# Performance work log

Hardware: AMD Instinct MI355X
Metric: run time of the kernel (lower is better)

The kernel has to match this reference:

```python
import jax, jax.numpy as jnp
import numpy as np


def silu(x):
    return x * jax.nn.sigmoid(x)


def setup_inputs() -> dict:
    key = jax.random.key(0)
    ks = jax.random.split(key, 16)
    b, n, k, d0, d1, hid = 2, 4096, 32, 64, 32, 32
    edge_in_dim = d0 * 2 + d1 + 1  # 161
    std = 1e-3  # init_eps normal init for Linear weights

    features0 = jax.random.normal(ks[0], (b, n, d0, 1), jnp.float32)
    features1 = jax.random.normal(ks[1], (b, n, d1, 3), jnp.float32)
    neighbor_indices = jax.random.randint(ks[2], (b, n, k), 0, n)
    neighbor_masks = jax.random.randint(ks[3], (b, n, k), 0, 2).astype(bool)
    rel_dist = jax.random.uniform(ks[4], (b, n, k), jnp.float32)

    def lin(kk, i, o):
        return std * jax.random.normal(kk, (i, o), jnp.float32)

    params = dict(
        W_e1=lin(ks[5], edge_in_dim, edge_in_dim * 2), b_e1=jnp.zeros(edge_in_dim * 2, jnp.float32),
        W_e2=lin(ks[6], edge_in_dim * 2, hid), b_e2=jnp.zeros(hid, jnp.float32),
        W_h1=lin(ks[7], hid, hid * 4), b_h1=jnp.zeros(hid * 4, jnp.float32),
        W_h2=lin(ks[8], hid * 4, d1), b_h2=jnp.zeros(d1, jnp.float32),
        W_n1=lin(ks[9], d0 + hid, d0 * 2), b_n1=jnp.zeros(d0 * 2, jnp.float32),
        W_n2=lin(ks[10], d0 * 2, d0), b_n2=jnp.zeros(d0, jnp.float32),
        W_g=lin(ks[11], d0, d1), b_g=jnp.zeros(d1, jnp.float32),
        ln_g=jnp.ones(d0, jnp.float32), ln_b=jnp.zeros(d0, jnp.float32),
        hn_scale=jnp.full((1, 1, 1, d1, 1), 0.01, jnp.float32),
        hn_bias=jnp.full((1, 1, 1, d1, 1), 0.01, jnp.float32),
    )
    return dict(features0=features0, features1=features1,
                neighbor_indices=neighbor_indices, neighbor_masks=neighbor_masks,
                rel_dist=rel_dist, **params)


def reference(features0, features1, neighbor_indices, neighbor_masks, rel_dist,
              W_e1, b_e1, W_e2, b_e2, W_h1, b_h1, W_h2, b_h2,
              W_n1, b_n1, W_n2, b_n2, W_g, b_g, ln_g, ln_b, hn_scale, hn_bias):
    b, n, k = neighbor_indices.shape
    bi = jnp.arange(b)[:, None, None]

    nodes = features0[..., 0]                                   # [b,n,d0]
    # gather neighbor higher-type features; rel_htype at selected pairs only
    h_j = features1[bi, neighbor_indices]                       # [b,n,k,d1,3]
    rel = features1[:, :, None, :, :] - h_j                     # [b,n,k,d1,3]
    rel_norm = jnp.linalg.norm(rel, axis=-1)                    # [b,n,k,d1]

    nodes_j = nodes[bi, neighbor_indices]                       # [b,n,k,d0]
    nodes_i = jnp.broadcast_to(nodes[:, :, None, :], nodes_j.shape)
    edge_in = jnp.concatenate([nodes_i, nodes_j, rel_norm, rel_dist[..., None]], axis=-1)

    m_ij = silu(silu(edge_in @ W_e1 + b_e1) @ W_e2 + b_e2)      # [b,n,k,hid]
    # NOTE: original splits htype_weights BEFORE masked_fill, so weights are unmasked
    w = silu(m_ij @ W_h1 + b_h1) @ W_h2 + b_h2                  # [b,n,k,d1]

    nrm = rel_norm[..., None]
    normed_rel = rel / jnp.clip(nrm, 1e-8) * (nrm * hn_scale + hn_bias)
    htype_update = jnp.einsum('bijdm,bijd->bidm', normed_rel, w)  # [b,n,d1,3]

    m_ij = jnp.where(neighbor_masks[..., None], m_ij, 0.0)
    m_i = m_ij.sum(axis=-2)                                     # [b,n,hid]

    mu = nodes.mean(-1, keepdims=True)
    var = nodes.var(-1, keepdims=True)
    normed_nodes = (nodes - mu) / jnp.sqrt(var + 1e-5) * ln_g + ln_b

    node_in = jnp.concatenate([normed_nodes, m_i], axis=-1)
    node_out = silu(node_in @ W_n1 + b_n1) @ W_n2 + b_n2 + nodes

    gate = jax.nn.sigmoid(node_out @ W_g + b_g)                 # [b,n,d1]
    f1_out = (features1 + htype_update) * gate[..., None]
    return node_out[..., None], f1_out
```

## Files before the change

### kernel.cpp

```cpp
#include <hip/hip_runtime.h>
#include <math.h>

#define NN_ 4096

typedef __attribute__((ext_vector_type(4))) float f4_t;
typedef __attribute__((ext_vector_type(2))) long l2_t;

__device__ __forceinline__ unsigned short f2bf(float x) {
    union { float f; unsigned u; } v; v.f = x;
    unsigned r = v.u + 0x7fffu + ((v.u >> 16) & 1u);
    return (unsigned short)(r >> 16);
}
__device__ __forceinline__ float bf2f(unsigned short h) {
    union { unsigned u; float f; } v; v.u = ((unsigned)h) << 16;
    return v.f;
}

__device__ __forceinline__ unsigned char sw_enc_fp8(float x) {
    if (x != x) return 0x7f;
    unsigned s = (x < 0.f) ? 0x80u : 0u;
    float a = fabsf(x);
    if (a >= 448.f) return (unsigned char)(s | 0x7e);
    int e; frexpf(a, &e); e -= 1;
    if (e < -6) e = -6;
    float scaled = ldexpf(a, 3 - e);
    int qq = (int)lrintf(scaled);
    if (qq >= 16) { qq = 8; e += 1; if (e > 8) return (unsigned char)(s | 0x7e); }
    if (qq < 8) return (unsigned char)(s | (unsigned)qq);
    return (unsigned char)(s | (unsigned)((e + 7) << 3) | (unsigned)(qq - 8));
}
__device__ __forceinline__ float sw_dec_fp8(unsigned char b) {
    int s = b >> 7, ef = (b >> 3) & 0xf, m = b & 7;
    float v = ef ? ldexpf((float)(8 + m), ef - 10) : ldexpf((float)m, -9);
    return s ? -v : v;
}
__device__ __forceinline__ unsigned pack4_fp8(float a, float b, float c, float d) {
#if __has_builtin(__builtin_amdgcn_cvt_pk_fp8_f32)
    int v = __builtin_amdgcn_cvt_pk_fp8_f32(a, b, 0, false);
    v = __builtin_amdgcn_cvt_pk_fp8_f32(c, d, v, true);
    return (unsigned)v;
#else
    return (unsigned)sw_enc_fp8(a) | ((unsigned)sw_enc_fp8(b) << 8) |
           ((unsigned)sw_enc_fp8(c) << 16) | ((unsigned)sw_enc_fp8(d) << 24);
#endif
}
__device__ __forceinline__ unsigned char enc_fp8(float a) {
#if __has_builtin(__builtin_amdgcn_cvt_pk_fp8_f32)
    return (unsigned char)(__builtin_amdgcn_cvt_pk_fp8_f32(a, 0.f, 0, false) & 0xff);
#else
    return sw_enc_fp8(a);
#endif
}
__device__ __forceinline__ float dec_fp8(unsigned char b) {
#if __has_builtin(__builtin_amdgcn_cvt_f32_fp8)
    return __builtin_amdgcn_cvt_f32_fp8((int)b, 0);
#else
    return sw_dec_fp8(b);
#endif
}
__device__ __forceinline__ f4_t mfma_fp8(long a, long b, f4_t c) {
    return __builtin_amdgcn_mfma_f32_16x16x32_fp8_fp8(a, b, c, 0, 0, 0);
}

__device__ __forceinline__ float silu_ps(float x, float S) {
    float x2 = x * x;
    float t = __builtin_fmaf(x2, -(S * (1.f / 48.f)), S * 0.25f);
    float s = __builtin_fmaf(x, t, S * 0.5f);
    return x * s;
}

#define WS_E2 67584
#define WS_H1 79872
#define WS_H2 83968
#define WS_N1 88064
#define WS_N2 100352
#define WS_G  108544
#define WS_END 110592

__global__ void __launch_bounds__(256) cvt_w(
    const float* __restrict__ W_e1, const float* __restrict__ W_e2,
    const float* __restrict__ W_h1, const float* __restrict__ W_h2,
    const float* __restrict__ W_n1, const float* __restrict__ W_n2,
    const float* __restrict__ W_g,  unsigned char* __restrict__ ws)
{
    int gid = blockIdx.x * 256 + threadIdx.x;
    if (gid >= WS_END) return;
    float v = 0.f;
    if (gid < WS_E2) {
        int t = gid / 3072, r = gid - t * 3072;
        int lane = r / 48; r -= lane * 48;
        int kc = r >> 3, b = r & 7;
        int n = t * 16 + (lane & 15), k = kc * 32 + (lane >> 4) * 8 + b;
        if (n < 322 && k < 161) v = W_e1[k * 322 + n];
    } else if (gid < WS_H1) {
        int g2 = gid - WS_E2;
        int mt = g2 / 6144; g2 -= mt * 6144;
        int lane = g2 / 96; g2 -= lane * 96;
        int s = g2 >> 3, b = g2 & 7;
        if (s < 11) {
            int n = mt * 16 + (lane & 15), k = s * 32 + (lane >> 4) * 8 + b;
            if (k < 322) v = W_e2[k * 32 + n];
        }
    } else if (gid < WS_H2) {
        int g2 = gid - WS_H1;
        int ng = g2 >> 11; g2 &= 2047;
        int lane = g2 >> 5, i = (g2 >> 3) & 3, b = g2 & 7;
        int n = (ng * 4 + i) * 16 + (lane & 15), k = (lane >> 4) * 8 + b;
        v = W_h1[k * 128 + n];
    } else if (gid < WS_N1) {
        int g2 = gid - WS_H2;
        int nt = g2 >> 11; g2 &= 2047;
        int lane = g2 >> 5, kc = (g2 >> 3) & 3, b = g2 & 7;
        int n = nt * 16 + (lane & 15), k = kc * 32 + (lane >> 4) * 8 + b;
        v = W_h2[k * 32 + n];
    } else if (gid < WS_N2) {
        int g2 = gid - WS_N1;
        int nt = g2 / 1536; g2 -= nt * 1536;
        int lane = g2 / 24; g2 -= lane * 24;
        int kc = g2 >> 3, b = g2 & 7;
        int n = nt * 16 + (lane & 15), k = kc * 32 + (lane >> 4) * 8 + b;
        v = W_n1[k * 128 + n];
    } else if (gid < WS_G) {
        int g2 = gid - WS_N2;
        int nt = g2 >> 11; g2 &= 2047;
        int lane = g2 >> 5, kc = (g2 >> 3) & 3, b = g2 & 7;
        int n = nt * 16 + (lane & 15), k = kc * 32 + (lane >> 4) * 8 + b;
        v = W_n2[k * 64 + n];
    } else {
        int g2 = gid - WS_G;
        int nt = g2 >> 10; g2 &= 1023;
        int lane = g2 >> 4, kc = (g2 >> 3) & 1, b = g2 & 7;
        int n = nt * 16 + (lane & 15), k = kc * 32 + (lane >> 4) * 8 + b;
        v = W_g[k * 32 + n];
    }
    ws[gid] = enc_fp8(v * 256.f);
}

__global__ void __launch_bounds__(256, 5) egnn_edge(
    const float* __restrict__ f0, const float* __restrict__ f1,
    const int* __restrict__ nidx, const int* __restrict__ nmsk,
    const float* __restrict__ rdist,
    const unsigned char* __restrict__ wbf,
    const float* __restrict__ b_e1, const float* __restrict__ b_e2,
    const float* __restrict__ b_h1, const float* __restrict__ b_h2,
    const float* __restrict__ hs,   const float* __restrict__ hb,
    float* __restrict__ out0, float* __restrict__ out1)
{
    __shared__ __align__(16) unsigned char R1[23040];
    __shared__ __align__(16) unsigned char R2[6144];
    __shared__ __align__(16) unsigned char R3[2560];
    __shared__ int s_jj[64];

    const int tid  = threadIdx.x;
    const int blk  = blockIdx.x;
    const int bb   = blk >> 11;
    const int wave = tid >> 6, lane = tid & 63;
    const int q    = lane >> 4, l16 = lane & 15;

    unsigned long long ball = 0;
    if (wave == 0) {
        int mv = nmsk[(size_t)blk * 64 + lane];
        ball = __ballot(mv != 0);
    }

    {
        const int e = tid >> 2, r = tid & 2 ? (tid & 3) : (tid & 3);
        const int rr4 = tid & 3;
        const int jj = nidx[(size_t)blk * 64 + e];
        if (rr4 == 0) s_jj[e] = jj;
        const int node = blk * 2 + (e >> 5);
        const float* ni = f0 + (size_t)node * 64;
        const float* nj = f0 + ((size_t)(bb * NN_ + jj)) * 64;
        const float* fi = f1 + (size_t)node * 96;
        const float* fj = f1 + ((size_t)(bb * NN_ + jj)) * 96;
        unsigned char* einp = R1 + e * 216;

        {
            float4 v0 = *(const float4*)(ni + 16 * rr4);
            float4 v1 = *(const float4*)(ni + 16 * rr4 + 4);
            float4 v2 = *(const float4*)(ni + 16 * rr4 + 8);
            float4 v3 = *(const float4*)(ni + 16 * rr4 + 12);
            uint2 w;
            w.x = pack4_fp8(v0.x, v0.y, v0.z, v0.w);
            w.y = pack4_fp8(v1.x, v1.y, v1.z, v1.w);
            *(uint2*)(einp + 16 * rr4) = w;
            w.x = pack4_fp8(v2.x, v2.y, v2.z, v2.w);
            w.y = pack4_fp8(v3.x, v3.y, v3.z, v3.w);
            *(uint2*)(einp + 16 * rr4 + 8) = w;
        }
        {
            float4 v0 = *(const float4*)(nj + 16 * rr4);
            float4 v1 = *(const float4*)(nj + 16 * rr4 + 4);
            float4 v2 = *(const float4*)(nj + 16 * rr4 + 8);
            float4 v3 = *(const float4*)(nj + 16 * rr4 + 12);
            uint2 w;
            w.x = pack4_fp8(v0.x, v0.y, v0.z, v0.w);
            w.y = pack4_fp8(v1.x, v1.y, v1.z, v1.w);
            *(uint2*)(einp + 64 + 16 * rr4) = w;
            w.x = pack4_fp8(v2.x, v2.y, v2.z, v2.w);
            w.y = pack4_fp8(v3.x, v3.y, v3.z, v3.w);
            *(uint2*)(einp + 64 + 16 * rr4 + 8) = w;
        }
        {
            float rl[24];
            #pragma unroll
            for (int s = 0; s < 6; s++) {
                float4 a = *(const float4*)(fi + 24 * rr4 + 4 * s);
                float4 c = *(const float4*)(fj + 24 * rr4 + 4 * s);
                rl[4*s+0] = a.x - c.x; rl[4*s+1] = a.y - c.y;
                rl[4*s+2] = a.z - c.z; rl[4*s+3] = a.w - c.w;
            }
            uint2* rdst = (uint2*)(R2 + e * 96 + 24 * rr4);
            uint2 u;
            u.x = pack4_fp8(rl[0], rl[1], rl[2],  rl[3]);
            u.y = pack4_fp8(rl[4], rl[5], rl[6],  rl[7]);
            rdst[0] = u;
            u.x = pack4_fp8(rl[8],  rl[9],  rl[10], rl[11]);
            u.y = pack4_fp8(rl[12], rl[13], rl[14], rl[15]);
            rdst[1] = u;
            u.x = pack4_fp8(rl[16], rl[17], rl[18], rl[19]);
            u.y = pack4_fp8(rl[20], rl[21], rl[22], rl[23]);
            rdst[2] = u;
            float nr[8];
            #pragma unroll
            for (int t = 0; t < 8; t++)
                nr[t] = __builtin_amdgcn_sqrtf(
                    __builtin_fmaf(rl[3*t], rl[3*t],
                    __builtin_fmaf(rl[3*t+1], rl[3*t+1], rl[3*t+2]*rl[3*t+2])));
            uint2 nw;
            nw.x = pack4_fp8(nr[0], nr[1], nr[2], nr[3]);
            nw.y = pack4_fp8(nr[4], nr[5], nr[6], nr[7]);
            *(uint2*)(einp + 128 + 8 * rr4) = nw;
        }
        if (rr4 == 0) {
            float rdv = rdist[(size_t)blk * 64 + e];
            uint2 w; w.x = pack4_fp8(rdv, 0.f, 0.f, 0.f); w.y = 0u;
            *(uint2*)(einp + 160) = w;
        } else {
            uint2 z; z.x = 0u; z.y = 0u;
            *(uint2*)(einp + 160 + 8 * rr4) = z;
        }
    }
    __syncthreads();

    long be[4][6];
    #pragma unroll
    for (int nt = 0; nt < 4; nt++) {
        const unsigned char* bp = R1 + ((nt * 16 + l16)) * 216 + q * 8;
        #pragma unroll
        for (int kc = 0; kc < 6; kc++)
            be[nt][kc] = *(const long*)(bp + kc * 32);
    }
    __syncthreads();

    for (int t = wave; t < 22; t += 4) {
        const unsigned char* wp = wbf + (size_t)t * 3072 + lane * 48;
        l2_t w0 = *(const l2_t*)(wp);
        l2_t w1 = *(const l2_t*)(wp + 16);
        l2_t w2 = *(const l2_t*)(wp + 32);
        long af[6] = {w0.x, w0.y, w1.x, w1.y, w2.x, w2.y};
        f4_t a0 = (f4_t)0.f, a1 = (f4_t)0.f, a2 = (f4_t)0.f, a3 = (f4_t)0.f;
        #pragma unroll
        for (int kc = 0; kc < 6; kc++) {
            a0 = mfma_fp8(af[kc], be[0][kc], a0);
            a1 = mfma_fp8(af[kc], be[1][kc], a1);
            a2 = mfma_fp8(af[kc], be[2][kc], a2);
            a3 = mfma_fp8(af[kc], be[3][kc], a3);
        }
        const int c0 = t * 16 + q * 4;
        float bv[4];
        if (c0 + 3 < 322) {
            float4 b4 = *(const float4*)(b_e1 + c0);
            bv[0] = b4.x; bv[1] = b4.y; bv[2] = b4.z; bv[3] = b4.w;
        } else {
            #pragma unroll
            for (int i = 0; i < 4; i++) bv[i] = (c0 + i < 322) ? b_e1[c0 + i] : 0.f;
        }
        #pragma unroll
        for (int nt = 0; nt < 4; nt++) {
            f4_t aa = nt == 0 ? a0 : (nt == 1 ? a1 : (nt == 2 ? a2 : a3));
            float y[4];
            #pragma unroll
            for (int i = 0; i < 4; i++) {
                float x = __builtin_fmaf(aa[i], 1.f / 256.f, bv[i]);
                y[i] = x * __builtin_fmaf(x, 16.f, 32.f);
            }
            *(unsigned*)(R1 + (nt * 16 + l16) * 360 + c0) =
                pack4_fp8(y[0], y[1], y[2], y[3]);
        }
    }
    __syncthreads();

    {
        const int mt2 = wave & 1;
        const unsigned char* wp2 = wbf + WS_E2 + mt2 * 6144 + lane * 96;
        long wf2[11];
        #pragma unroll
        for (int p = 0; p < 5; p++) {
            l2_t u = *(const l2_t*)(wp2 + p * 16);
            wf2[2 * p] = u.x; wf2[2 * p + 1] = u.y;
        }
        wf2[10] = *(const long*)(wp2 + 80);
        int h0 = mt2 * 16 + q * 4;
        float4 b4 = *(const float4*)(b_e2 + h0);
        float bvv[4] = {b4.x, b4.y, b4.z, b4.w};
        #pragma unroll
        for (int half = 0; half < 2; half++) {
            const int ntile = (wave >> 1) + half * 2;
            long ba[11];
            const unsigned char* apb = R1 + (ntile * 16 + l16) * 360 + q * 8;
            #pragma unroll
            for (int kc = 0; kc < 11; kc++) ba[kc] = *(const long*)(apb + kc * 32);
            f4_t m0 = (f4_t)0.f;
            #pragma unroll
            for (int kc = 0; kc < 11; kc++)
                m0 = mfma_fp8(wf2[kc], ba[kc], m0);
            const int e = ntile * 16 + l16;
            float y[4];
            #pragma unroll
            for (int i = 0; i < 4; i++) {
                float x = __builtin_fmaf(m0[i], 1.f / 16384.f, bvv[i]);
                y[i] = x * __builtin_fmaf(x, 2048.f, 4096.f);
            }
            *(unsigned*)(R3 + e * 40 + h0) = pack4_fp8(y[0], y[1], y[2], y[3]);
        }
    }
    __syncthreads();

    {
        const int em = wave;
        long am = *(const long*)(R3 + (em * 16 + l16) * 40 + q * 8);
        #pragma unroll
        for (int ng = 0; ng < 2; ng++) {
            const unsigned char* hp = wbf + WS_H1 + ng * 2048 + lane * 32;
            l2_t hv0 = *(const l2_t*)hp;
            l2_t hv1 = *(const l2_t*)(hp + 16);
            long bw[4] = {hv0.x, hv0.y, hv1.x, hv1.y};
            #pragma unroll
            for (int i = 0; i < 4; i++) {
                int nt = ng * 4 + i;
                f4_t a3 = mfma_fp8(am, bw[i], (f4_t)0.f);
                int c = nt * 16 + l16;
                float bv = b_h1[c];
                #pragma unroll
                for (int rr = 0; rr < 4; rr++) {
                    int e = em * 16 + q * 4 + rr;
                    float zh = __builtin_fmaf(a3[rr], 1.f / 2097152.f, bv);
                    R1[e * 152 + c] = enc_fp8(silu_ps(zh, 4194304.f));
                }
            }
        }
    }
    __syncthreads();

    {
        const int em = wave;
        const unsigned char* ap = R1 + (em * 16 + l16) * 152 + q * 8;
        long aq[4];
        #pragma unroll
        for (int kc = 0; kc < 4; kc++) aq[kc] = *(const long*)(ap + kc * 32);
        unsigned short* wfp = (unsigned short*)(R1 + 16384);
        #pragma unroll
        for (int nt2 = 0; nt2 < 2; nt2++) {
            const unsigned char* wp = wbf + WS_H2 + nt2 * 2048 + lane * 32;
            l2_t wv0 = *(const l2_t*)wp;
            l2_t wv1 = *(const l2_t*)(wp + 16);
            f4_t cc = (f4_t)0.f;
            cc = mfma_fp8(aq[0], wv0.x, cc);
            cc = mfma_fp8(aq[1], wv0.y, cc);
            cc = mfma_fp8(aq[2], wv1.x, cc);
            cc = mfma_fp8(aq[3], wv1.y, cc);
            int d = nt2 * 16 + l16;
            float bv = b_h2[d], hss = hs[d], hbb = hb[d];
            #pragma unroll
            for (int rr = 0; rr < 4; rr++) {
                int e = em * 16 + q * 4 + rr;
                float r0 = dec_fp8(R2[e * 96 + 3 * d + 0]);
                float r1 = dec_fp8(R2[e * 96 + 3 * d + 1]);
                float r2 = dec_fp8(R2[e * 96 + 3 * d + 2]);
                float nr = __builtin_amdgcn_sqrtf(
                    __builtin_fmaf(r0, r0, __builtin_fmaf(r1, r1, r2 * r2)));
                float fac = __builtin_fmaf(nr, hss, hbb) *
                            __builtin_amdgcn_rcpf(fmaxf(nr, 1e-8f));
                float wout = __builtin_fmaf(cc[rr], 1.f / 1073741824.f, bv);
                wfp[e * 36 + d] = f2bf(wout * fac);
            }
        }
    }
    __syncthreads();

    const unsigned short* wfp = (const unsigned short*)(R1 + 16384);
    #pragma unroll
    for (int sel = 0; sel < 2; sel++) {
        const int node = blk * 2 + sel;
        if (wave == 0) {
            const int hq = lane & 7, g = lane >> 3;
            float a0 = 0.f, a1 = 0.f, a2 = 0.f, a3 = 0.f;
            #pragma unroll
            for (int it = 0; it < 4; it++) {
                int e = sel * 32 + g * 4 + it;
                float mf = ((ball >> e) & 1ull) ? 1.f : 0.f;
                unsigned m4 = *(const unsigned*)(R3 + e * 40 + hq * 4);
                a0 = __builtin_fmaf(mf, dec_fp8((unsigned char)(m4 & 0xff)), a0);
                a1 = __builtin_fmaf(mf, dec_fp8((unsigned char)((m4 >> 8) & 0xff)), a1);
                a2 = __builtin_fmaf(mf, dec_fp8((unsigned char)((m4 >> 16) & 0xff)), a2);
                a3 = __builtin_fmaf(mf, dec_fp8((unsigned char)(m4 >> 24)), a3);
            }
            #pragma unroll
            for (int m = 8; m <= 32; m <<= 1) {
                a0 += __shfl_xor(a0, m);
                a1 += __shfl_xor(a1, m);
                a2 += __shfl_xor(a2, m);
                a3 += __shfl_xor(a3, m);
            }
            if (g == 0) {
                float4 o;
                o.x = a0 * (1.f / 8192.f); o.y = a1 * (1.f / 8192.f);
                o.z = a2 * (1.f / 8192.f); o.w = a3 * (1.f / 8192.f);
                *(float4*)(out0 + (size_t)node * 64 + 32 + hq * 4) = o;
            }
        } else {
            const int jj = (wave - 1) * 32 + (lane & 31);
            const int gh = lane >> 5;
            const int dd = (jj * 21846) >> 16;
            const int qr = (lane & 31) >> 2;
            float acc = 0.f;
            #pragma unroll
            for (int it = 0; it < 16; it++) {
                int e = sel * 32 + gh * 16 + ((it + qr) & 15);
                float rv = dec_fp8(R2[e * 96 + jj]);
                float wv = bf2f(wfp[e * 36 + dd]);
                acc = __builtin_fmaf(rv, wv, acc);
            }
            acc += __shfl_xor(acc, 32);
            if (lane < 32) out1[(size_t)node * 96 + jj] = acc;
        }
    }
}

__global__ void __launch_bounds__(256, 4) egnn_node(
    const float* __restrict__ f0, const float* __restrict__ f1,
    const unsigned char* __restrict__ wbf,
    const float* __restrict__ b_n1, const float* __restrict__ b_n2,
    const float* __restrict__ b_g,
    const float* __restrict__ ln_g, const float* __restrict__ ln_b,
    float* __restrict__ out0, float* __restrict__ out1)
{
    __shared__ __align__(8) unsigned char s_in[8 * 104];
    __shared__ __align__(8) unsigned char s_n1[8 * 136];
    __shared__ __align__(8) unsigned char s_no[8 * 72];
    __shared__ float s_f0[8 * 68];
    __shared__ float s_gate[8 * 32];

    const int tid  = threadIdx.x;
    const int r0   = blockIdx.x * 8;
    const int wave = tid >> 6, lane = tid & 63;
    const int q    = lane >> 4, l16 = lane & 15;

    {
        int rr = tid >> 5, c = (tid & 31) * 2;
        float2 v = *(const float2*)(f0 + (size_t)(r0 + rr) * 64 + c);
        *(float2*)(s_f0 + rr * 68 + c) = v;
    }
    __syncthreads();

    {
        int row = tid >> 5, sub = tid & 31;
        const float* rp = s_f0 + row * 68 + sub * 2;
        float x0 = rp[0], x1 = rp[1];
        float s = x0 + x1, s2 = x0 * x0 + x1 * x1;
        #pragma unroll
        for (int m = 1; m < 32; m <<= 1) {
            s  += __shfl_xor(s, m);
            s2 += __shfl_xor(s2, m);
        }
        float mu = s * (1.f / 64.f);
        float rstd = rsqrtf(s2 * (1.f / 64.f) - mu * mu + 1e-5f);
        int c0 = sub * 2;
        float y0 = (x0 - mu) * rstd * ln_g[c0] + ln_b[c0];
        float y1 = (x1 - mu) * rstd * ln_g[c0 + 1] + ln_b[c0 + 1];
        unsigned pv = (unsigned)enc_fp8(y0) | ((unsigned)enc_fp8(y1) << 8);
        *(unsigned short*)(s_in + row * 104 + c0) = (unsigned short)pv;
    }
    if (tid < 64) {
        int r = tid >> 3, h4 = (tid & 7) * 4;
        float4 v = *(const float4*)(out0 + (size_t)(r0 + r) * 64 + 32 + h4);
        *(unsigned*)(s_in + r * 104 + 64 + h4) = pack4_fp8(v.x, v.y, v.z, v.w);
    }
    __syncthreads();

    {
        long af[3];
        #pragma unroll
        for (int kc = 0; kc < 3; kc++)
            af[kc] = *(const long*)(s_in + l16 * 104 + kc * 32 + q * 8);
        #pragma unroll
        for (int i = 0; i < 2; i++) {
            int nt = wave * 2 + i;
            const unsigned char* wp = wbf + WS_N1 + nt * 1536 + lane * 24;
            long w0 = *(const long*)(wp);
            long w1 = *(const long*)(wp + 8);
            long w2 = *(const long*)(wp + 16);
            f4_t acc = (f4_t)0.f;
            acc = mfma_fp8(af[0], w0, acc);
            acc = mfma_fp8(af[1], w1, acc);
            acc = mfma_fp8(af[2], w2, acc);
            int col = nt * 16 + l16;
            float bv = b_n1[col];
            #pragma unroll
            for (int rr = 0; rr < 4; rr++) {
                int row = q * 4 + rr;
                if (row < 8) {
                    float x = __builtin_fmaf(acc[rr], 1.f / 256.f, bv);
                    s_n1[row * 136 + col] = enc_fp8(silu_ps(x, 64.f));
                }
            }
        }
    }
    __syncthreads();

    {
        long af[4];
        #pragma unroll
        for (int kc = 0; kc < 4; kc++)
            af[kc] = *(const long*)(s_n1 + l16 * 136 + kc * 32 + q * 8);
        const unsigned char* wp = wbf + WS_N2 + wave * 2048 + lane * 32;
        l2_t w01 = *(const l2_t*)wp;
        l2_t w23 = *(const l2_t*)(wp + 16);
        long bw[4] = {w01.x, w01.y, w23.x, w23.y};
        f4_t acc = (f4_t)0.f;
        #pragma unroll
        for (int kc = 0; kc < 4; kc++) acc = mfma_fp8(af[kc], bw[kc], acc);
        int col = wave * 16 + l16;
        float bv = b_n2[col];
        #pragma unroll
        for (int rr = 0; rr < 4; rr++) {
            int row = q * 4 + rr;
            if (row < 8) {
                float no = __builtin_fmaf(acc[rr], 1.f / 16384.f, bv) + s_f0[row * 68 + col];
                out0[(size_t)(r0 + row) * 64 + col] = no;
                s_no[row * 72 + col] = enc_fp8(no);
            }
        }
    }
    __syncthreads();

    if (wave < 2) {
        long a0 = *(const long*)(s_no + l16 * 72 + q * 8);
        long a1 = *(const long*)(s_no + l16 * 72 + 32 + q * 8);
        const unsigned char* wp = wbf + WS_G + wave * 1024 + lane * 16;
        l2_t w = *(const l2_t*)wp;
        f4_t acc = (f4_t)0.f;
        acc = mfma_fp8(a0, w.x, acc);
        acc = mfma_fp8(a1, w.y, acc);
        int d = wave * 16 + l16;
        float bv = b_g[d];
        #pragma unroll
        for (int rr = 0; rr < 4; rr++) {
            int row = q * 4 + rr;
            if (row < 8) {
                float x = __builtin_fmaf(acc[rr], 1.f / 256.f, bv);
                float x2 = x * x;
                s_gate[row * 32 + d] =
                    __builtin_fmaf(x, __builtin_fmaf(x2, -(1.f / 48.f), 0.25f), 0.5f);
            }
        }
    }
    __syncthreads();

    if (tid < 64) {
        int n = tid >> 3, j = (tid & 7) * 12;
        size_t base = (size_t)(r0 + n) * 96 + j;
        float4 fa = *(const float4*)(f1 + base);
        float4 fb = *(const float4*)(f1 + base + 4);
        float4 fc = *(const float4*)(f1 + base + 8);
        float4 ha = *(const float4*)(out1 + base);
        float4 hb4 = *(const float4*)(out1 + base + 4);
        float4 hc = *(const float4*)(out1 + base + 8);
        const float* gp = s_gate + n * 32 + (j / 3);
        float g0 = gp[0], g1 = gp[1], g2 = gp[2], g3 = gp[3];
        float4 o0, o1, o2;
        o0.x = (fa.x + ha.x) * g0; o0.y = (fa.y + ha.y) * g0;
        o0.z = (fa.z + ha.z) * g0; o0.w = (fa.w + ha.w) * g1;
        o1.x = (fb.x + hb4.x) * g1; o1.y = (fb.y + hb4.y) * g1;
        o1.z = (fb.z + hb4.z) * g2; o1.w = (fb.w + hb4.w) * g2;
        o2.x = (fc.x + hc.x) * g2; o2.y = (fc.y + hc.y) * g3;
        o2.z = (fc.z + hc.z) * g3; o2.w = (fc.w + hc.w) * g3;
        *(float4*)(out1 + base)     = o0;
        *(float4*)(out1 + base + 4) = o1;
        *(float4*)(out1 + base + 8) = o2;
    }
}

extern "C" void kernel_launch(void* const* d_in, const int* in_sizes, int n_in,
                              void* d_out, int out_size, void* d_ws, size_t ws_size,
                              hipStream_t stream) {
    const float* f0   = (const float*)d_in[0];
    const float* f1   = (const float*)d_in[1];
    const int*   nidx = (const int*)d_in[2];
    const int*   nmsk = (const int*)d_in[3];
    const float* rd   = (const float*)d_in[4];
    const float* W_e1 = (const float*)d_in[5];
    const float* b_e1 = (const float*)d_in[6];
    const float* W_e2 = (const float*)d_in[7];
    const float* b_e2 = (const float*)d_in[8];
    const float* W_h1 = (const float*)d_in[9];
    const float* b_h1 = (const float*)d_in[10];
    const float* W_h2 = (const float*)d_in[11];
    const float* b_h2 = (const float*)d_in[12];
    const float* W_n1 = (const float*)d_in[13];
    const float* b_n1 = (const float*)d_in[14];
    const float* W_n2 = (const float*)d_in[15];
    const float* b_n2 = (const float*)d_in[16];
    const float* W_g  = (const float*)d_in[17];
    const float* b_g  = (const float*)d_in[18];
    const float* ln_g = (const float*)d_in[19];
    const float* ln_b = (const float*)d_in[20];
    const float* hs   = (const float*)d_in[21];
    const float* hb   = (const float*)d_in[22];

    unsigned char* wbf = (unsigned char*)d_ws;
    float* out0 = (float*)d_out;
    float* out1 = out0 + (size_t)2 * NN_ * 64;

    cvt_w<<<432, 256, 0, stream>>>(W_e1, W_e2, W_h1, W_h2, W_n1, W_n2, W_g, wbf);
    egnn_edge<<<NN_, 256, 0, stream>>>(
        f0, f1, nidx, nmsk, rd, wbf,
        b_e1, b_e2, b_h1, b_h2, hs, hb, out0, out1);
    egnn_node<<<2 * NN_ / 8, 256, 0, stream>>>(
        f0, f1, wbf, b_n1, b_n2, b_g, ln_g, ln_b, out0, out1);
}
```

Before: 171.3 us.

## Split first edge GEMM into two halves to shrink LDS and raise occupancy

```diff
diff --git a/kernel.cpp b/kernel.cpp
--- a/kernel.cpp
+++ b/kernel.cpp
@@ -136,7 +136,7 @@
     ws[gid] = enc_fp8(v * 256.f);
 }
 
-__global__ void __launch_bounds__(256, 5) egnn_edge(
+__global__ void __launch_bounds__(256, 6) egnn_edge(
     const float* __restrict__ f0, const float* __restrict__ f1,
     const int* __restrict__ nidx, const int* __restrict__ nmsk,
     const float* __restrict__ rdist,
@@ -146,10 +146,10 @@
     const float* __restrict__ hs,   const float* __restrict__ hb,
     float* __restrict__ out0, float* __restrict__ out1)
 {
-    __shared__ __align__(16) unsigned char R1[23040];
+    __shared__ __align__(16) unsigned char R1[13824];
     __shared__ __align__(16) unsigned char R2[6144];
     __shared__ __align__(16) unsigned char R3[2560];
-    __shared__ int s_jj[64];
+    __shared__ __align__(16) unsigned char WF[4608];
 
     const int tid  = threadIdx.x;
     const int blk  = blockIdx.x;
@@ -164,10 +164,8 @@
     }
 
     {
-        const int e = tid >> 2, r = tid & 2 ? (tid & 3) : (tid & 3);
-        const int rr4 = tid & 3;
+        const int e = tid >> 2, rr4 = tid & 3;
         const int jj = nidx[(size_t)blk * 64 + e];
-        if (rr4 == 0) s_jj[e] = jj;
         const int node = blk * 2 + (e >> 5);
         const float* ni = f0 + (size_t)node * 64;
         const float* nj = f0 + ((size_t)(bb * NN_ + jj)) * 64;
@@ -243,29 +241,81 @@
     }
     __syncthreads();
 
-    long be[4][6];
+    const int nd = wave >> 1;
+    long be[2][6];
     #pragma unroll
-    for (int nt = 0; nt < 4; nt++) {
-        const unsigned char* bp = R1 + ((nt * 16 + l16)) * 216 + q * 8;
+    for (int nt2 = 0; nt2 < 2; nt2++) {
+        const unsigned char* bp = R1 + ((nd * 2 + nt2) * 16 + l16) * 216 + q * 8;
         #pragma unroll
         for (int kc = 0; kc < 6; kc++)
-            be[nt][kc] = *(const long*)(bp + kc * 32);
-    }
-    __syncthreads();
-
-    for (int t = wave; t < 22; t += 4) {
+            be[nt2][kc] = *(const long*)(bp + kc * 32);
+    }
+    __syncthreads();
+
+    for (int t = (wave & 1); t < 12; t += 2) {
         const unsigned char* wp = wbf + (size_t)t * 3072 + lane * 48;
         l2_t w0 = *(const l2_t*)(wp);
         l2_t w1 = *(const l2_t*)(wp + 16);
         l2_t w2 = *(const l2_t*)(wp + 32);
         long af[6] = {w0.x, w0.y, w1.x, w1.y, w2.x, w2.y};
-        f4_t a0 = (f4_t)0.f, a1 = (f4_t)0.f, a2 = (f4_t)0.f, a3 = (f4_t)0.f;
+        f4_t a0 = (f4_t)0.f, a1 = (f4_t)0.f;
         #pragma unroll
         for (int kc = 0; kc < 6; kc++) {
             a0 = mfma_fp8(af[kc], be[0][kc], a0);
             a1 = mfma_fp8(af[kc], be[1][kc], a1);
-            a2 = mfma_fp8(af[kc], be[2][kc], a2);
-            a3 = mfma_fp8(af[kc], be[3][kc], a3);
+        }
+        const int c0 = t * 16 + q * 4;
+        float4 b4 = *(const float4*)(b_e1 + c0);
+        float bv[4] = {b4.x, b4.y, b4.z, b4.w};
+        #pragma unroll
+        for (int nt2 = 0; nt2 < 2; nt2++) {
+            f4_t aa = nt2 ? a1 : a0;
+            float y[4];
+            #pragma unroll
+            for (int i = 0; i < 4; i++) {
+                float x = __builtin_fmaf(aa[i], 1.f / 256.f, bv[i]);
+                y[i] = x * __builtin_fmaf(x, 16.f, 32.f);
+            }
+            *(unsigned*)(R1 + ((nd * 2 + nt2) * 16 + l16) * 216 + c0) =
+                pack4_fp8(y[0], y[1], y[2], y[3]);
+        }
+    }
+    __syncthreads();
+
+    const int mt2 = wave & 1;
+    const unsigned char* wp2 = wbf + WS_E2 + mt2 * 6144 + lane * 96;
+    f4_t m0[2];
+    {
+        l2_t u0 = *(const l2_t*)(wp2);
+        l2_t u1 = *(const l2_t*)(wp2 + 16);
+        l2_t u2 = *(const l2_t*)(wp2 + 32);
+        long wf[6] = {u0.x, u0.y, u1.x, u1.y, u2.x, u2.y};
+        #pragma unroll
+        for (int half = 0; half < 2; half++) {
+            const int ntile = (wave >> 1) + half * 2;
+            const unsigned char* apb = R1 + (ntile * 16 + l16) * 216 + q * 8;
+            long ba[6];
+            #pragma unroll
+            for (int kc = 0; kc < 6; kc++) ba[kc] = *(const long*)(apb + kc * 32);
+            f4_t acc = (f4_t)0.f;
+            #pragma unroll
+            for (int kc = 0; kc < 6; kc++) acc = mfma_fp8(wf[kc], ba[kc], acc);
+            m0[half] = acc;
+        }
+    }
+    __syncthreads();
+
+    for (int t = 12 + (wave & 1); t < 22; t += 2) {
+        const unsigned char* wp = wbf + (size_t)t * 3072 + lane * 48;
+        l2_t w0 = *(const l2_t*)(wp);
+        l2_t w1 = *(const l2_t*)(wp + 16);
+        l2_t w2 = *(const l2_t*)(wp + 32);
+        long af[6] = {w0.x, w0.y, w1.x, w1.y, w2.x, w2.y};
+        f4_t a0 = (f4_t)0.f, a1 = (f4_t)0.f;
+        #pragma unroll
+        for (int kc = 0; kc < 6; kc++) {
+            a0 = mfma_fp8(af[kc], be[0][kc], a0);
+            a1 = mfma_fp8(af[kc], be[1][kc], a1);
         }
         const int c0 = t * 16 + q * 4;
         float bv[4];
@@ -277,49 +327,43 @@
             for (int i = 0; i < 4; i++) bv[i] = (c0 + i < 322) ? b_e1[c0 + i] : 0.f;
         }
         #pragma unroll
-        for (int nt = 0; nt < 4; nt++) {
-            f4_t aa = nt == 0 ? a0 : (nt == 1 ? a1 : (nt == 2 ? a2 : a3));
+        for (int nt2 = 0; nt2 < 2; nt2++) {
+            f4_t aa = nt2 ? a1 : a0;
             float y[4];
             #pragma unroll
             for (int i = 0; i < 4; i++) {
                 float x = __builtin_fmaf(aa[i], 1.f / 256.f, bv[i]);
                 y[i] = x * __builtin_fmaf(x, 16.f, 32.f);
             }
-            *(unsigned*)(R1 + (nt * 16 + l16) * 360 + c0) =
+            *(unsigned*)(R1 + ((nd * 2 + nt2) * 16 + l16) * 216 + (c0 - 192)) =
                 pack4_fp8(y[0], y[1], y[2], y[3]);
         }
     }
     __syncthreads();
 
     {
-        const int mt2 = wave & 1;
-        const unsigned char* wp2 = wbf + WS_E2 + mt2 * 6144 + lane * 96;
-        long wf2[11];
-        #pragma unroll
-        for (int p = 0; p < 5; p++) {
-            l2_t u = *(const l2_t*)(wp2 + p * 16);
-            wf2[2 * p] = u.x; wf2[2 * p + 1] = u.y;
-        }
-        wf2[10] = *(const long*)(wp2 + 80);
-        int h0 = mt2 * 16 + q * 4;
+        l2_t v0 = *(const l2_t*)(wp2 + 48);
+        l2_t v1 = *(const l2_t*)(wp2 + 64);
+        long w10 = *(const long*)(wp2 + 80);
+        long wf[5] = {v0.x, v0.y, v1.x, v1.y, w10};
+        const int h0 = mt2 * 16 + q * 4;
         float4 b4 = *(const float4*)(b_e2 + h0);
         float bvv[4] = {b4.x, b4.y, b4.z, b4.w};
         #pragma unroll
         for (int half = 0; half < 2; half++) {
             const int ntile = (wave >> 1) + half * 2;
-            long ba[11];
-            const unsigned char* apb = R1 + (ntile * 16 + l16) * 360 + q * 8;
-            #pragma unroll
-            for (int kc = 0; kc < 11; kc++) ba[kc] = *(const long*)(apb + kc * 32);
-            f4_t m0 = (f4_t)0.f;
-            #pragma unroll
-            for (int kc = 0; kc < 11; kc++)
-                m0 = mfma_fp8(wf2[kc], ba[kc], m0);
+            const unsigned char* apb = R1 + (ntile * 16 + l16) * 216 + q * 8;
+            long ba[5];
+            #pragma unroll
+            for (int j = 0; j < 5; j++) ba[j] = *(const long*)(apb + j * 32);
+            f4_t acc = m0[half];
+            #pragma unroll
+            for (int j = 0; j < 5; j++) acc = mfma_fp8(wf[j], ba[j], acc);
             const int e = ntile * 16 + l16;
             float y[4];
             #pragma unroll
             for (int i = 0; i < 4; i++) {
-                float x = __builtin_fmaf(m0[i], 1.f / 16384.f, bvv[i]);
+                float x = __builtin_fmaf(acc[i], 1.f / 16384.f, bvv[i]);
                 y[i] = x * __builtin_fmaf(x, 2048.f, 4096.f);
             }
             *(unsigned*)(R3 + e * 40 + h0) = pack4_fp8(y[0], y[1], y[2], y[3]);
@@ -330,6 +374,7 @@
     {
         const int em = wave;
         long am = *(const long*)(R3 + (em * 16 + l16) * 40 + q * 8);
+        const int e = em * 16 + l16;
         #pragma unroll
         for (int ng = 0; ng < 2; ng++) {
             const unsigned char* hp = wbf + WS_H1 + ng * 2048 + lane * 32;
@@ -338,16 +383,15 @@
             long bw[4] = {hv0.x, hv0.y, hv1.x, hv1.y};
             #pragma unroll
             for (int i = 0; i < 4; i++) {
-                int nt = ng * 4 + i;
-                f4_t a3 = mfma_fp8(am, bw[i], (f4_t)0.f);
-                int c = nt * 16 + l16;
-                float bv = b_h1[c];
-                #pragma unroll
-                for (int rr = 0; rr < 4; rr++) {
-                    int e = em * 16 + q * 4 + rr;
-                    float zh = __builtin_fmaf(a3[rr], 1.f / 2097152.f, bv);
-                    R1[e * 152 + c] = enc_fp8(silu_ps(zh, 4194304.f));
-                }
+                f4_t a3 = mfma_fp8(bw[i], am, (f4_t)0.f);
+                int c0 = (ng * 4 + i) * 16 + q * 4;
+                float4 b4 = *(const float4*)(b_h1 + c0);
+                float y[4];
+                y[0] = silu_ps(__builtin_fmaf(a3[0], 1.f / 2097152.f, b4.x), 4194304.f);
+                y[1] = silu_ps(__builtin_fmaf(a3[1], 1.f / 2097152.f, b4.y), 4194304.f);
+                y[2] = silu_ps(__builtin_fmaf(a3[2], 1.f / 2097152.f, b4.z), 4194304.f);
+                y[3] = silu_ps(__builtin_fmaf(a3[3], 1.f / 2097152.f, b4.w), 4194304.f);
+                *(unsigned*)(R1 + e * 152 + c0) = pack4_fp8(y[0], y[1], y[2], y[3]);
             }
         }
     }
@@ -359,7 +403,7 @@
         long aq[4];
         #pragma unroll
         for (int kc = 0; kc < 4; kc++) aq[kc] = *(const long*)(ap + kc * 32);
-        unsigned short* wfp = (unsigned short*)(R1 + 16384);
+        unsigned short* wfp = (unsigned short*)WF;
         #pragma unroll
         for (int nt2 = 0; nt2 < 2; nt2++) {
             const unsigned char* wp = wbf + WS_H2 + nt2 * 2048 + lane * 32;
@@ -389,7 +433,7 @@
     }
     __syncthreads();
 
-    const unsigned short* wfp = (const unsigned short*)(R1 + 16384);
+    const unsigned short* wfp = (const unsigned short*)WF;
     #pragma unroll
     for (int sel = 0; sel < 2; sel++) {
         const int node = blk * 2 + sel;
```

Result: slower. 192.3 us (+12.3%).
